# Performance work log

Measured on AMD Instinct MI355X. Metric: run time of the kernel, lower is better.

## Reference

```python
import jax, jax.numpy as jnp
import numpy as np

B, T, S = 8, 96, 192          # batch, tgt_len (decoder steps), src_len (encoder memory)
D_IN, D_MEM = 512, 512        # input_size (query dim), mem_size (memory dim)


def setup_inputs() -> dict:
    key = jax.random.key(0)
    ks = jax.random.split(key, 9)
    w = 0.02  # init scale for learned params
    inputs = jax.random.normal(ks[0], (B, T, D_IN), jnp.float32)
    mems = jax.random.normal(ks[1], (B, S, D_MEM), jnp.float32)
    # lengths in [1, S] so no row is fully masked
    mem_masks = jax.random.randint(ks[2], (B,), 1, S + 1)
    Wq = jax.random.normal(ks[3], (D_MEM, D_IN), jnp.float32) * w    # linear_q.weight (no bias)
    Wc = jax.random.normal(ks[4], (D_MEM, D_MEM), jnp.float32) * w   # linear_c.weight
    bc = jax.random.normal(ks[5], (D_MEM,), jnp.float32) * w         # linear_c.bias
    v = jax.random.normal(ks[6], (D_MEM,), jnp.float32) * w          # v.weight (mem_size -> 1)
    Wout = jax.random.normal(ks[7], (D_IN, D_MEM + D_IN), jnp.float32) * w  # linear_out.weight
    bout = jax.random.normal(ks[8], (D_IN,), jnp.float32) * w        # linear_out.bias
    return dict(inputs=inputs, mems=mems, mem_masks=mem_masks,
                Wq=Wq, Wc=Wc, bc=bc, v=v, Wout=Wout, bout=bout)


def reference(inputs, mems, mem_masks, Wq, Wc, bc, v, Wout, bout):
    # score(): additive (tanh-MLP) attention
    wq = jnp.einsum('btd,md->btm', inputs, Wq)          # [B,T,Dm]
    uh = jnp.einsum('bsd,md->bsm', mems, Wc) + bc        # [B,S,Dm]
    # broadcast-add -> tanh -> project with v : [B,T,S]
    align = jnp.einsum('btsm,m->bts', jnp.tanh(wq[:, :, None, :] + uh[:, None, :, :]), v)
    # sequence_mask from lengths, applied along src dim
    mask = jnp.arange(S) < mem_masks[:, None]            # [B,S] bool
    align = jnp.where(mask[:, None, :], align, -jnp.inf)
    align_vectors = jax.nn.softmax(align, axis=-1)       # [B,T,S]
    c = jnp.einsum('bts,bsd->btd', align_vectors, mems)  # context [B,T,Dm]
    attn_h = jnp.concatenate([c, inputs], axis=-1) @ Wout.T + bout  # [B,T,D_IN]
    return attn_h, align_vectors
```

## Files before the change

### kernel.cpp

```cpp
#include <hip/hip_runtime.h>
#include <math.h>

#define BB 8
#define TT 96
#define SS 192
#define DIN 512
#define DM 512

typedef short short8 __attribute__((ext_vector_type(8)));
typedef float f32x4 __attribute__((ext_vector_type(4)));

__device__ __forceinline__ unsigned short f2bf(float f) {
    unsigned int u = __float_as_uint(f);
    unsigned int r = u + 0x7FFFu + ((u >> 16) & 1u);
    return (unsigned short)(r >> 16);
}
__device__ __forceinline__ float bf2f(unsigned short h) {
    return __uint_as_float(((unsigned int)h) << 16);
}

__device__ __forceinline__ void load_lds16(const void* g, void* l) {
    __builtin_amdgcn_global_load_lds((__attribute__((address_space(1))) void*)g,
                                     (__attribute__((address_space(3))) void*)l,
                                     16, 0, 0);
}

__global__ __launch_bounds__(256) void prep_cvt(
    const float* __restrict__ s0, const float* __restrict__ s1,
    const float* __restrict__ s2, const float* __restrict__ s3,
    const float* __restrict__ s4,
    unsigned short* __restrict__ d0, unsigned short* __restrict__ d1,
    unsigned short* __restrict__ d2, unsigned short* __restrict__ d3,
    unsigned short* __restrict__ d4)
{
    int bid = blockIdx.x;
    const float* s; unsigned short* d; int base;
    if (bid < 192)      { s = s0; d = d0; base = bid * 2048; }
    else if (bid < 576) { s = s1; d = d1; base = (bid - 192) * 2048; }
    else if (bid < 704) { s = s2; d = d2; base = (bid - 576) * 2048; }
    else if (bid < 832) { s = s3; d = d3; base = (bid - 704) * 2048; }
    else                { s = s4; d = d4; base = (bid - 832) * 2048; }
    int idx = base + threadIdx.x * 8;
    float4 a = *(const float4*)(s + idx);
    float4 b = *(const float4*)(s + idx + 4);
    short8 o;
    o[0] = (short)f2bf(a.x); o[1] = (short)f2bf(a.y);
    o[2] = (short)f2bf(a.z); o[3] = (short)f2bf(a.w);
    o[4] = (short)f2bf(b.x); o[5] = (short)f2bf(b.y);
    o[6] = (short)f2bf(b.z); o[7] = (short)f2bf(b.w);
    *(short8*)(d + idx) = o;
}

__device__ __forceinline__ void gemm_tile(
    unsigned short* As, unsigned short* Ws,
    const unsigned short* __restrict__ A, int lda,
    const unsigned short* __restrict__ W, int ldw,
    const float* __restrict__ bias,
    float* __restrict__ outF, unsigned short* __restrict__ outB,
    int bm, int bn, int N, int K)
{
    const int tid = threadIdx.x;
    const int r  = tid >> 2;
    const int kc = (tid & 3) * 8;
    const int lane = tid & 63, wv = tid >> 6;
    const int quad = lane >> 4, mrow = lane & 15;

    f32x4 acc0 = {0,0,0,0}, acc1 = {0,0,0,0}, acc2 = {0,0,0,0}, acc3 = {0,0,0,0};

    const unsigned short* arow = A + (size_t)(bm + r) * lda;
    const unsigned short* wrow = W + (size_t)(bn + r) * ldw;

    load_lds16(arow + kc, As + tid * 8);
    load_lds16(wrow + kc, Ws + tid * 8);
    __syncthreads();

    const int NC = K >> 5;
    for (int c = 0; c < NC; ++c) {
        const int cur = (c & 1) * 2048;
        if (c + 1 < NC) {
            const int nxt = 2048 - cur;
            int gk = ((c + 1) << 5) + kc;
            load_lds16(arow + gk, As + nxt + tid * 8);
            load_lds16(wrow + gk, Ws + nxt + tid * 8);
        }
        short8 av = *(const short8*)(As + cur + (wv * 16 + mrow) * 32 + quad * 8);
        short8 b0 = *(const short8*)(Ws + cur + (mrow) * 32 + quad * 8);
        short8 b1 = *(const short8*)(Ws + cur + (16 + mrow) * 32 + quad * 8);
        short8 b2 = *(const short8*)(Ws + cur + (32 + mrow) * 32 + quad * 8);
        short8 b3 = *(const short8*)(Ws + cur + (48 + mrow) * 32 + quad * 8);
        acc0 = __builtin_amdgcn_mfma_f32_16x16x32_bf16(av, b0, acc0, 0, 0, 0);
        acc1 = __builtin_amdgcn_mfma_f32_16x16x32_bf16(av, b1, acc1, 0, 0, 0);
        acc2 = __builtin_amdgcn_mfma_f32_16x16x32_bf16(av, b2, acc2, 0, 0, 0);
        acc3 = __builtin_amdgcn_mfma_f32_16x16x32_bf16(av, b3, acc3, 0, 0, 0);
        __syncthreads();
    }

    f32x4 accs[4] = {acc0, acc1, acc2, acc3};
    #pragma unroll
    for (int ct = 0; ct < 4; ++ct) {
        int col = bn + ct * 16 + mrow;
        float bv = bias ? bias[col] : 0.0f;
        #pragma unroll
        for (int rg = 0; rg < 4; ++rg) {
            int rw = bm + wv * 16 + quad * 4 + rg;
            float val = accs[ct][rg] + bv;
            if (outF) outF[(size_t)rw * N + col] = val;
            else      outB[(size_t)rw * N + col] = f2bf(val);
        }
    }
}

__global__ __launch_bounds__(256) void proj_gemm(
    const unsigned short* __restrict__ inputs_bf,
    const unsigned short* __restrict__ mems_bf,
    const unsigned short* __restrict__ Wq_bf,
    const unsigned short* __restrict__ Wc_bf,
    const float* __restrict__ bc,
    const unsigned short* __restrict__ Wout_bf,
    const float* __restrict__ bout,
    unsigned short* __restrict__ wq_o, unsigned short* __restrict__ uh_o,
    unsigned short* __restrict__ m2_o, float* __restrict__ ih_o)
{
    __shared__ __align__(16) unsigned short As[2 * 2048];
    __shared__ __align__(16) unsigned short Ws[2 * 2048];
    int bid = blockIdx.x;
    if (bid < 96) {
        gemm_tile(As, Ws, inputs_bf, DIN, Wq_bf, DIN, nullptr, nullptr, wq_o,
                  (bid >> 3) * 64, (bid & 7) * 64, DM, DIN);
    } else if (bid < 288) {
        bid -= 96;
        gemm_tile(As, Ws, mems_bf, DM, Wc_bf, DM, bc, nullptr, uh_o,
                  (bid >> 3) * 64, (bid & 7) * 64, DM, DM);
    } else if (bid < 480) {
        bid -= 288;
        gemm_tile(As, Ws, mems_bf, DM, Wout_bf, DM + DIN, nullptr, nullptr, m2_o,
                  (bid >> 3) * 64, (bid & 7) * 64, DM, DM);
    } else {
        bid -= 480;
        gemm_tile(As, Ws, inputs_bf, DIN, Wout_bf + DM, DM + DIN, bout, ih_o, nullptr,
                  (bid >> 3) * 64, (bid & 7) * 64, DIN, DIN);
    }
}

__global__ __launch_bounds__(256) void attn_core(
    const unsigned short* __restrict__ wq,
    const unsigned short* __restrict__ uh,
    const float* __restrict__ v,
    const unsigned short* __restrict__ m2,
    const float* __restrict__ ih,
    const int* __restrict__ masks,
    float* __restrict__ align_out,
    float* __restrict__ attn_h)
{
    __shared__ float s_align[SS];
    __shared__ __align__(16) float s_part[4][DM];
    __shared__ float s_stat;
    const int row = blockIdx.x, b = row / TT;
    const int tid = threadIdx.x, lane = tid & 63, wid = tid >> 6;
    const int len = masks[b];

    float qf[8], vf[8];
    {
        short8 q = *(const short8*)(wq + (size_t)row * DM + lane * 8);
        float4 v0 = *(const float4*)(v + lane * 8);
        float4 v1 = *(const float4*)(v + lane * 8 + 4);
        #pragma unroll
        for (int j = 0; j < 8; ++j) qf[j] = bf2f((unsigned short)q[j]);
        vf[0] = v0.x; vf[1] = v0.y; vf[2] = v0.z; vf[3] = v0.w;
        vf[4] = v1.x; vf[5] = v1.y; vf[6] = v1.z; vf[7] = v1.w;
    }

    for (int s = wid; s < SS; s += 4) {
        float val = -INFINITY;
        if (s < len) {
            short8 u = *(const short8*)(uh + ((size_t)b * SS + s) * DM + lane * 8);
            float part = 0.f;
            #pragma unroll
            for (int j = 0; j < 8; ++j) {
                float x = qf[j] + bf2f((unsigned short)u[j]);
                float e = __builtin_amdgcn_exp2f(x * 2.885390082f);
                float th = fmaf(-2.f, __builtin_amdgcn_rcpf(e + 1.f), 1.f);
                part = fmaf(vf[j], th, part);
            }
            #pragma unroll
            for (int off = 32; off; off >>= 1)
                part += __shfl_xor(part, off);
            val = part;
        }
        if (lane == 0) s_align[s] = val;
    }
    __syncthreads();

    if (tid < 64) {
        float m = fmaxf(fmaxf(s_align[tid], s_align[tid + 64]), s_align[tid + 128]);
        #pragma unroll
        for (int off = 32; off; off >>= 1) m = fmaxf(m, __shfl_xor(m, off));
        float e0 = __builtin_amdgcn_exp2f((s_align[tid]       - m) * 1.44269504f);
        float e1 = __builtin_amdgcn_exp2f((s_align[tid + 64]  - m) * 1.44269504f);
        float e2 = __builtin_amdgcn_exp2f((s_align[tid + 128] - m) * 1.44269504f);
        s_align[tid] = e0; s_align[tid + 64] = e1; s_align[tid + 128] = e2;
        float sum = e0 + e1 + e2;
        #pragma unroll
        for (int off = 32; off; off >>= 1) sum += __shfl_xor(sum, off);
        if (tid == 0) s_stat = 1.0f / sum;
    }
    __syncthreads();
    const float inv = s_stat;
    if (tid < SS) align_out[(size_t)row * SS + tid] = s_align[tid] * inv;

    float accv[8] = {0,0,0,0,0,0,0,0};
    const unsigned short* m2b = m2 + ((size_t)b * SS + wid * 48) * DM + lane * 8;
    #pragma unroll 8
    for (int i = 0; i < 48; ++i) {
        float p = s_align[wid * 48 + i];
        short8 mv = *(const short8*)(m2b + (size_t)i * DM);
        #pragma unroll
        for (int j = 0; j < 8; ++j)
            accv[j] = fmaf(p, bf2f((unsigned short)mv[j]), accv[j]);
    }
    {
        float4 t0; t0.x = accv[0]; t0.y = accv[1]; t0.z = accv[2]; t0.w = accv[3];
        float4 t1; t1.x = accv[4]; t1.y = accv[5]; t1.z = accv[6]; t1.w = accv[7];
        *(float4*)&s_part[wid][lane * 8]     = t0;
        *(float4*)&s_part[wid][lane * 8 + 4] = t1;
    }
    __syncthreads();

    const int d0 = tid * 2;
    float r0 = s_part[0][d0]     + s_part[1][d0]     + s_part[2][d0]     + s_part[3][d0];
    float r1 = s_part[0][d0 + 1] + s_part[1][d0 + 1] + s_part[2][d0 + 1] + s_part[3][d0 + 1];
    float2 ihv = *(const float2*)(ih + (size_t)row * DIN + d0);
    float2 o;
    o.x = fmaf(r0, inv, ihv.x);
    o.y = fmaf(r1, inv, ihv.y);
    *(float2*)(attn_h + (size_t)row * DIN + d0) = o;
}

extern "C" void kernel_launch(void* const* d_in, const int* in_sizes, int n_in,
                              void* d_out, int out_size, void* d_ws, size_t ws_size,
                              hipStream_t stream) {
    (void)in_sizes; (void)n_in; (void)out_size; (void)ws_size;
    const float* inputs = (const float*)d_in[0];
    const float* mems   = (const float*)d_in[1];
    const int*   masks  = (const int*)  d_in[2];
    const float* Wq     = (const float*)d_in[3];
    const float* Wc     = (const float*)d_in[4];
    const float* bc     = (const float*)d_in[5];
    const float* v      = (const float*)d_in[6];
    const float* Wout   = (const float*)d_in[7];
    const float* bout   = (const float*)d_in[8];

    unsigned short* p = (unsigned short*)d_ws;
    unsigned short* inputs_bf = p;        p += 393216;
    unsigned short* mems_bf   = p;        p += 786432;
    unsigned short* Wq_bf     = p;        p += 262144;
    unsigned short* Wc_bf     = p;        p += 262144;
    unsigned short* Wout_bf   = p;        p += 524288;
    unsigned short* uh_bf     = p;        p += 786432;
    unsigned short* wq_bf     = p;        p += 393216;
    unsigned short* m2_bf     = p;        p += 786432;
    float* ih                 = (float*)p;

    float* attn_h    = (float*)d_out;
    float* align_out = attn_h + (size_t)BB * TT * DIN;

    prep_cvt<<<1088, 256, 0, stream>>>(inputs, mems, Wq, Wc, Wout,
                                       inputs_bf, mems_bf, Wq_bf, Wc_bf, Wout_bf);
    proj_gemm<<<576, 256, 0, stream>>>(inputs_bf, mems_bf, Wq_bf, Wc_bf, bc,
                                       Wout_bf, bout, wq_bf, uh_bf, m2_bf, ih);
    attn_core<<<BB * TT, 256, 0, stream>>>(wq_bf, uh_bf, v, m2_bf, ih, masks,
                                           align_out, attn_h);
}
```

Baseline: 119.4 us.

## Triple-buffer projection GEMM LDS loads with explicit vmcnt waits

Moves the projection GEMM tile loop from double to triple buffering in LDS, prefetching two K-chunks ahead. It replaces __syncthreads with explicit s_waitcnt vmcnt and raw s_barrier plus sched_barrier, so more global loads stay in flight while the MFMAs run. This costs extra LDS per block and depends on the hand-counted vmcnt values being correct. The projection kernel is only one part of the whole pipeline, so any effect on total time may be small.

```diff
diff --git a/kernel.cpp b/kernel.cpp
--- a/kernel.cpp
+++ b/kernel.cpp
@@ -70,29 +70,41 @@
     const unsigned short* arow = A + (size_t)(bm + r) * lda;
     const unsigned short* wrow = W + (size_t)(bn + r) * ldw;
 
-    load_lds16(arow + kc, As + tid * 8);
-    load_lds16(wrow + kc, Ws + tid * 8);
-    __syncthreads();
+    load_lds16(arow + kc,      As + tid * 8);
+    load_lds16(wrow + kc,      Ws + tid * 8);
+    load_lds16(arow + 32 + kc, As + 2048 + tid * 8);
+    load_lds16(wrow + 32 + kc, Ws + 2048 + tid * 8);
 
     const int NC = K >> 5;
+    int cur = 0;
     for (int c = 0; c < NC; ++c) {
-        const int cur = (c & 1) * 2048;
-        if (c + 1 < NC) {
-            const int nxt = 2048 - cur;
-            int gk = ((c + 1) << 5) + kc;
-            load_lds16(arow + gk, As + nxt + tid * 8);
-            load_lds16(wrow + gk, Ws + nxt + tid * 8);
+        if (c + 2 < NC) {
+            int nb = cur + 2; if (nb >= 3) nb -= 3;
+            int gk = ((c + 2) << 5) + kc;
+            load_lds16(arow + gk, As + nb * 2048 + tid * 8);
+            load_lds16(wrow + gk, Ws + nb * 2048 + tid * 8);
+            asm volatile("s_waitcnt vmcnt(4)" ::: "memory");
+        } else if (c + 1 < NC) {
+            asm volatile("s_waitcnt vmcnt(2)" ::: "memory");
+        } else {
+            asm volatile("s_waitcnt vmcnt(0)" ::: "memory");
         }
-        short8 av = *(const short8*)(As + cur + (wv * 16 + mrow) * 32 + quad * 8);
-        short8 b0 = *(const short8*)(Ws + cur + (mrow) * 32 + quad * 8);
-        short8 b1 = *(const short8*)(Ws + cur + (16 + mrow) * 32 + quad * 8);
-        short8 b2 = *(const short8*)(Ws + cur + (32 + mrow) * 32 + quad * 8);
-        short8 b3 = *(const short8*)(Ws + cur + (48 + mrow) * 32 + quad * 8);
+        __builtin_amdgcn_s_barrier();
+        __builtin_amdgcn_sched_barrier(0);
+        const unsigned short* Ab = As + cur * 2048;
+        const unsigned short* Wb = Ws + cur * 2048;
+        short8 av = *(const short8*)(Ab + (wv * 16 + mrow) * 32 + quad * 8);
+        short8 b0 = *(const short8*)(Wb + (mrow) * 32 + quad * 8);
+        short8 b1 = *(const short8*)(Wb + (16 + mrow) * 32 + quad * 8);
+        short8 b2 = *(const short8*)(Wb + (32 + mrow) * 32 + quad * 8);
+        short8 b3 = *(const short8*)(Wb + (48 + mrow) * 32 + quad * 8);
         acc0 = __builtin_amdgcn_mfma_f32_16x16x32_bf16(av, b0, acc0, 0, 0, 0);
         acc1 = __builtin_amdgcn_mfma_f32_16x16x32_bf16(av, b1, acc1, 0, 0, 0);
         acc2 = __builtin_amdgcn_mfma_f32_16x16x32_bf16(av, b2, acc2, 0, 0, 0);
         acc3 = __builtin_amdgcn_mfma_f32_16x16x32_bf16(av, b3, acc3, 0, 0, 0);
-        __syncthreads();
+        __builtin_amdgcn_sched_barrier(0);
+        __builtin_amdgcn_s_barrier();
+        cur += 1; if (cur >= 3) cur -= 3;
     }
 
     f32x4 accs[4] = {acc0, acc1, acc2, acc3};
@@ -121,8 +133,8 @@
     unsigned short* __restrict__ wq_o, unsigned short* __restrict__ uh_o,
     unsigned short* __restrict__ m2_o, float* __restrict__ ih_o)
 {
-    __shared__ __align__(16) unsigned short As[2 * 2048];
-    __shared__ __align__(16) unsigned short Ws[2 * 2048];
+    __shared__ __align__(16) unsigned short As[3 * 2048];
+    __shared__ __align__(16) unsigned short Ws[3 * 2048];
     int bid = blockIdx.x;
     if (bid < 96) {
         gemm_tile(As, Ws, inputs_bf, DIN, Wq_bf, DIN, nullptr, nullptr, wq_o,
```

Measured after the change: 117.6 us. About the same (-1.5%).
